# Kernel tuning notes

Measured on AMD Instinct MI355X. Metric: run time of the kernel, lower is better.

## Reference

```python
import jax, jax.numpy as jnp
import numpy as np

BS, N, D, B, D_PM = 8, 4096, 1024, 8, 64
BUDGET = 16.0


def setup_inputs() -> dict:
    key = jax.random.key(0)
    ks = jax.random.split(key, 6)
    H = jax.random.normal(ks[0], (BS, N, D), jnp.float32)
    surprise = jax.random.normal(ks[1], (BS, N, D), jnp.float32)
    # W_pm initialized as (1/B)*I + small noise, as in initialize()
    eye = jnp.eye(D_PM, dtype=jnp.float32)
    W_pm = eye / B + 0.01 * jax.random.normal(ks[2], (BS, B, D_PM, D_PM), jnp.float32)
    proj_in_w = jax.random.normal(ks[3], (D_PM, D), jnp.float32) / np.float32(np.sqrt(D))
    proj_in_b = jnp.zeros((D_PM,), jnp.float32)
    # original zero-inits proj_out; use small values so output is non-trivial
    proj_out_w = 0.02 * jax.random.normal(ks[4], (D, D_PM), jnp.float32)
    proj_out_b = jnp.zeros((D,), jnp.float32)
    raw_beta = jnp.full((B,), -3.0, jnp.float32)
    raw_decay = jnp.full((B,), np.float32(np.log(0.999 / 0.001)), jnp.float32)  # logit(0.999)
    surp_scale = jnp.ones((1,), jnp.float32)
    surp_bias = jnp.zeros((1,), jnp.float32)
    return dict(H=H, surprise=surprise, W_pm=W_pm,
                proj_in_w=proj_in_w, proj_in_b=proj_in_b,
                proj_out_w=proj_out_w, proj_out_b=proj_out_b,
                raw_beta=raw_beta, raw_decay=raw_decay,
                surp_scale=surp_scale, surp_bias=surp_bias)


def reference(H, surprise, W_pm, proj_in_w, proj_in_b, proj_out_w, proj_out_b,
              raw_beta, raw_decay, surp_scale, surp_bias):
    # ---- read ----
    pre = jnp.einsum('bnd,pd->bnp', H, proj_in_w) + proj_in_b          # [BS,N,D_pm]
    W_sum = jnp.sum(W_pm, axis=1)                                      # [BS,D_pm,D_pm]
    post = jnp.einsum('bnp,bqp->bnq', pre, W_sum)                      # pre @ W_sum^T
    pm_read = jnp.einsum('bnq,dq->bnd', post, proj_out_w) + proj_out_b # [BS,N,D]
    # ---- commit (Hebbian, surprise-gated) ----
    surp_mag = jnp.linalg.norm(surprise, axis=-1)                      # [BS,N]
    s = jax.nn.sigmoid(surp_scale * surp_mag + surp_bias)              # [BS,N]
    weighted = jnp.sqrt(s)[..., None] * pre                            # [BS,N,D_pm]
    G = jnp.einsum('bnp,bnq->bpq', weighted, weighted) / N             # [BS,D_pm,D_pm]
    beta = jax.nn.softplus(raw_beta)                                   # [B]
    decay = jax.nn.sigmoid(raw_decay)                                  # [B]
    eye = jnp.eye(D_PM, dtype=pre.dtype)
    T = decay[None, :, None, None] * eye + beta[None, :, None, None] * G[:, None]  # [BS,B,D_pm,D_pm]
    W_new = jnp.einsum('bkij,bkjq->bkiq', W_pm, T)                     # [BS,B,D_pm,D_pm]
    frob = jnp.sqrt(jnp.sum(W_new * W_new, axis=(-2, -1), keepdims=True))
    scale = jnp.minimum(BUDGET / jnp.maximum(frob, 1e-8), 1.0)
    W_new = W_new * scale
    return pm_read, W_new
```

## Files before the change

kernel.cpp:

```cpp
#include <hip/hip_runtime.h>

typedef unsigned short u16;
typedef unsigned int u32;
typedef __attribute__((ext_vector_type(4))) float f32x4;
typedef __attribute__((ext_vector_type(8))) short s16x8;

static constexpr int N_ = 4096;
static constexpr int D_ = 1024;

#define WAITV(N) asm volatile("s_waitcnt vmcnt(" #N ")" ::: "memory")
#define MEMCLOB() asm volatile("" ::: "memory")

__device__ __forceinline__ u16 f2bf(float f) {
  unsigned u = __float_as_uint(f);
  u += 0x7FFFu + ((u >> 16) & 1u);
  return (u16)(u >> 16);
}

__device__ __forceinline__ f32x4 zero4() {
  f32x4 z; z[0] = 0.f; z[1] = 0.f; z[2] = 0.f; z[3] = 0.f; return z;
}

__device__ __forceinline__ void gload16(const void* g, void* lds) {
  __builtin_amdgcn_global_load_lds(
      (const __attribute__((address_space(1))) u32*)g,
      (__attribute__((address_space(3))) u32*)lds, 16, 0, 0);
}

__global__ __launch_bounds__(256) void k_aux(
    const float* __restrict__ Wpm, const float* __restrict__ piw,
    const float* __restrict__ pw, u16* __restrict__ WpB,
    u16* __restrict__ MB) {
  __shared__ float Ws[64][65];
  int bid = blockIdx.x, tid = threadIdx.x;
  if (bid < 16) {
    size_t i0 = (size_t)bid * 4096;
    for (int idx = tid; idx < 4096; idx += 256)
      WpB[i0 + idx] = f2bf(piw[i0 + idx]);
    return;
  }
  int idx2 = bid - 16;
  int b = idx2 >> 4, t = idx2 & 15;
  for (int idx = tid; idx < 4096; idx += 256) {
    float s = 0.f;
#pragma unroll
    for (int k = 0; k < 8; ++k)
      s += Wpm[((size_t)(b * 8 + k)) * 4096 + idx];
    Ws[idx >> 6][idx & 63] = s;
  }
  __syncthreads();
  u16* mb = MB + ((size_t)b << 16);
  for (int oidx = tid; oidx < 4096; oidx += 256) {
    int r = oidx >> 6, c = oidx & 63;
    int drow = t * 64 + r;
    const float* prow = pw + (size_t)drow * 64;
    float acc = 0.f;
#pragma unroll 8
    for (int q = 0; q < 64; ++q) acc += prow[q] * Ws[q][c];
    mb[(size_t)drow * 64 + c] = f2bf(acc);
  }
}

__global__ __launch_bounds__(512, 4) void k_main(
    const float* __restrict__ H, const float* __restrict__ Sur,
    const float* __restrict__ pib, const float* __restrict__ pob,
    const float* __restrict__ sscale_p, const float* __restrict__ sbias_p,
    const u16* __restrict__ WpB, const u16* __restrict__ MB,
    float* __restrict__ Gpart, float* __restrict__ out) {
  __shared__ __align__(16) char arena[65536];
  __shared__ float sqsL[64];

  const int tid = threadIdx.x;
  const int lane = tid & 63;
  const int w = tid >> 6;
  const int wm = w & 3;
  const int wk = w >> 2;
  const int llo = lane & 15;
  const int lhi = lane >> 4;
  const int b = blockIdx.x >> 6;
  const int row0 = (blockIdx.x & 63) * 64;

  {
    const float* sb = Sur + ((size_t)b * N_ + row0) * D_;
    const float sscale = sscale_p[0], sbias = sbias_p[0];
#pragma unroll
    for (int g = 0; g < 2; ++g) {
      const float4* r0 = (const float4*)(sb + (size_t)(w * 8 + g * 4) * D_) + lane;
      float s0 = 0.f, s1 = 0.f, s2 = 0.f, s3 = 0.f;
#pragma unroll
      for (int c = 0; c < 4; ++c) {
        float4 v0 = r0[c * 64];
        float4 v1 = r0[256 + c * 64];
        float4 v2 = r0[512 + c * 64];
        float4 v3 = r0[768 + c * 64];
        s0 += v0.x * v0.x + v0.y * v0.y + v0.z * v0.z + v0.w * v0.w;
        s1 += v1.x * v1.x + v1.y * v1.y + v1.z * v1.z + v1.w * v1.w;
        s2 += v2.x * v2.x + v2.y * v2.y + v2.z * v2.z + v2.w * v2.w;
        s3 += v3.x * v3.x + v3.y * v3.y + v3.z * v3.z + v3.w * v3.w;
      }
#pragma unroll
      for (int m = 1; m < 64; m <<= 1) {
        s0 += __shfl_xor(s0, m, 64);
        s1 += __shfl_xor(s1, m, 64);
        s2 += __shfl_xor(s2, m, 64);
        s3 += __shfl_xor(s3, m, 64);
      }
      float res = s0;
      if (lane == 1) res = s1;
      if (lane == 2) res = s2;
      if (lane == 3) res = s3;
      if (lane < 4) {
        float mag = sqrtf(res);
        float s = 1.f / (1.f + __expf(-(sscale * mag + sbias)));
        sqsL[w * 8 + g * 4 + lane] = sqrtf(s);
      }
    }
  }
  __syncthreads();

  const int srow = 8 * w + (lane >> 3);
  const int sc16 = (lane & 7) ^ (srow & 7);
  const float* hsrc = H + ((size_t)b * N_ + row0 + srow) * D_ + sc16 * 4;
  const u16* wpb = WpB + (size_t)wk * 512 + lhi * 8;

  f32x4 accA[4];
#pragma unroll
  for (int t = 0; t < 4; ++t) accA[t] = zero4();
  s16x8 Bf[2][4];

  const int arow = wm * 16 + llo;
  const int r7a = arow & 7;

#define STAGEH(kc)                                                          \
  gload16(hsrc + (kc) * 32, arena + ((kc) & 3) * 16384 + w * 1024);         \
  gload16(hsrc + 512 + (kc) * 32, arena + ((kc) & 3) * 16384 + 8192 + w * 1024)

#define LOADB(kc)                                                           \
  _Pragma("unroll") for (int t = 0; t < 4; ++t) Bf[(kc) & 1][t] =           \
      *(const s16x8*)(wpb + (size_t)(t * 16 + llo) * 1024 + (kc) * 32)

  STAGEH(0); STAGEH(1); STAGEH(2);
  LOADB(0); LOADB(1);
  MEMCLOB();

#pragma unroll
  for (int kc = 0; kc < 16; ++kc) {
    if (kc <= 13) { WAITV(12); }
    else if (kc == 14) { WAITV(8); }
    else { WAITV(0); }
    __builtin_amdgcn_s_barrier();
    MEMCLOB();
    {
      const char* abase = arena + (kc & 3) * 16384 + wk * 8192 + arow * 128;
      f32x4 alo = *(const f32x4*)(abase + (((lhi * 2) ^ r7a) * 16));
      f32x4 ahi = *(const f32x4*)(abase + (((lhi * 2 + 1) ^ r7a) * 16));
      s16x8 af;
      af[0] = (short)f2bf(alo[0]); af[1] = (short)f2bf(alo[1]);
      af[2] = (short)f2bf(alo[2]); af[3] = (short)f2bf(alo[3]);
      af[4] = (short)f2bf(ahi[0]); af[5] = (short)f2bf(ahi[1]);
      af[6] = (short)f2bf(ahi[2]); af[7] = (short)f2bf(ahi[3]);
#pragma unroll
      for (int t = 0; t < 4; ++t)
        accA[t] = __builtin_amdgcn_mfma_f32_16x16x32_bf16(af, Bf[kc & 1][t],
                                                          accA[t], 0, 0, 0);
    }
    if (kc + 2 < 16) { LOADB(kc + 2); }
    if (kc + 3 < 16) { STAGEH(kc + 3); }
    MEMCLOB();
  }
#undef STAGEH
#undef LOADB

  float bias_t[4];
#pragma unroll
  for (int t = 0; t < 4; ++t) bias_t[t] = pib[t * 16 + llo];

  __syncthreads();
  float (*preF)[65] = (float(*)[65])arena;
  u16 (*preRP)[72] = (u16(*)[72])(arena + 18432);
  u16 (*wRPT)[72] = (u16(*)[72])(arena + 28672);
  float* pobL = (float*)(arena + 38912);

  if (wk == 1) {
#pragma unroll
    for (int t = 0; t < 4; ++t)
#pragma unroll
      for (int r = 0; r < 4; ++r)
        preF[wm * 16 + lhi * 4 + r][t * 16 + llo] = accA[t][r];
  }
  __syncthreads();
  if (wk == 0) {
#pragma unroll
    for (int t = 0; t < 4; ++t)
#pragma unroll
      for (int r = 0; r < 4; ++r) {
        int row = wm * 16 + lhi * 4 + r;
        float v = accA[t][r] + preF[row][t * 16 + llo] + bias_t[t];
        preRP[row][t * 16 + llo] = f2bf(v);
        wRPT[t * 16 + llo][row] = f2bf(v * sqsL[row]);
      }
  }
  __syncthreads();

  {
    f32x4 accG[4];
#pragma unroll
    for (int t = 0; t < 4; ++t) accG[t] = zero4();
    s16x8 ag = *(const s16x8*)&wRPT[wm * 16 + llo][wk * 32 + lhi * 8];
#pragma unroll
    for (int t = 0; t < 4; ++t) {
      s16x8 bg = *(const s16x8*)&wRPT[t * 16 + llo][wk * 32 + lhi * 8];
      accG[t] = __builtin_amdgcn_mfma_f32_16x16x32_bf16(ag, bg, accG[t], 0, 0, 0);
    }
    float* gout = Gpart + ((size_t)blockIdx.x * 2 + wk) * 4096;
#pragma unroll
    for (int t = 0; t < 4; ++t)
#pragma unroll
      for (int r = 0; r < 4; ++r)
        gout[(wm * 16 + lhi * 4 + r) * 64 + t * 16 + llo] = accG[t][r];
  }
  pobL[tid] = pob[tid];
  pobL[tid + 512] = pob[tid + 512];
  __syncthreads();

  {
    s16x8 ad0 = *(const s16x8*)&preRP[wm * 16 + llo][lhi * 8];
    s16x8 ad1 = *(const s16x8*)&preRP[wm * 16 + llo][32 + lhi * 8];
    const u16* mcol = MB + ((size_t)b << 16) + (size_t)(wk * 512) * 64 + lhi * 8;
    float* orow = out + ((size_t)b * N_ + row0 + wm * 16) * D_;
#pragma unroll
    for (int c = 0; c < 8; ++c) {
      s16x8 f0[4], f1[4];
#pragma unroll
      for (int i = 0; i < 4; ++i) {
        const u16* p = mcol + (size_t)(c * 64 + i * 16 + llo) * 64;
        f0[i] = *(const s16x8*)p;
        f1[i] = *(const s16x8*)(p + 32);
      }
#pragma unroll
      for (int i = 0; i < 4; ++i) {
        f32x4 acc = zero4();
        acc = __builtin_amdgcn_mfma_f32_16x16x32_bf16(ad0, f0[i], acc, 0, 0, 0);
        acc = __builtin_amdgcn_mfma_f32_16x16x32_bf16(ad1, f1[i], acc, 0, 0, 0);
        int n0 = wk * 512 + c * 64 + i * 16;
        float bias = pobL[n0 + llo];
#pragma unroll
        for (int r = 0; r < 4; ++r)
          orow[(size_t)(lhi * 4 + r) * D_ + n0 + llo] = acc[r] + bias;
      }
    }
  }
}

__global__ __launch_bounds__(256) void k_gred(
    const float* __restrict__ Gpart, float* __restrict__ Gsum) {
  __shared__ float red[4][64];
  int b = blockIdx.x >> 6, g = blockIdx.x & 63;
  int lane = threadIdx.x & 63, q = threadIdx.x >> 6;
  const float* src = Gpart + ((size_t)b * 128 + q * 32) * 4096 + g * 64 + lane;
  float s = 0.f;
#pragma unroll 8
  for (int i = 0; i < 32; ++i) s += src[(size_t)i * 4096];
  red[q][lane] = s;
  __syncthreads();
  if (q == 0)
    Gsum[(size_t)b * 4096 + g * 64 + lane] =
        red[0][lane] + red[1][lane] + red[2][lane] + red[3][lane];
}

__global__ __launch_bounds__(256) void k_wnew(
    const float* __restrict__ Wpm, const float* __restrict__ Gsum,
    const float* __restrict__ rbeta, const float* __restrict__ rdecay,
    float* __restrict__ outW) {
  __shared__ float Wk[64][66];
  __shared__ float Gl[64][66];
  __shared__ float red[4];
  int bk = blockIdx.x;
  int b = bk >> 3, k = bk & 7;
  int tid = threadIdx.x;
  const float* wsrc = Wpm + (size_t)bk * 4096;
  const float* gsrc = Gsum + (size_t)b * 4096;
  for (int idx = tid; idx < 4096; idx += 256) {
    Wk[idx >> 6][idx & 63] = wsrc[idx];
    Gl[idx >> 6][idx & 63] = gsrc[idx];
  }
  __syncthreads();
  float beta = log1pf(__expf(rbeta[k]));
  float decay = 1.f / (1.f + __expf(-rdecay[k]));
  float bn = beta * (1.f / 4096.f);
  int q = tid & 63;
  int rbase = tid >> 6;
  float vals[16];
  float ss = 0.f;
#pragma unroll
  for (int i = 0; i < 16; ++i) {
    int row = i * 4 + rbase;
    float acc = 0.f;
#pragma unroll 8
    for (int j = 0; j < 64; ++j) acc += Wk[row][j] * Gl[j][q];
    float v = decay * Wk[row][q] + bn * acc;
    vals[i] = v;
    ss += v * v;
  }
#pragma unroll
  for (int m = 1; m < 64; m <<= 1) ss += __shfl_xor(ss, m, 64);
  if ((tid & 63) == 0) red[tid >> 6] = ss;
  __syncthreads();
  float frob = sqrtf(red[0] + red[1] + red[2] + red[3]);
  float scale = fminf(16.f / fmaxf(frob, 1e-8f), 1.f);
  float* dst = outW + (size_t)bk * 4096;
#pragma unroll
  for (int i = 0; i < 16; ++i) dst[i * 256 + tid] = vals[i] * scale;
}

extern "C" void kernel_launch(void* const* d_in, const int* in_sizes, int n_in,
                              void* d_out, int out_size, void* d_ws, size_t ws_size,
                              hipStream_t stream) {
  const float* H      = (const float*)d_in[0];
  const float* Sur    = (const float*)d_in[1];
  const float* Wpm    = (const float*)d_in[2];
  const float* piw    = (const float*)d_in[3];
  const float* pib    = (const float*)d_in[4];
  const float* pw     = (const float*)d_in[5];
  const float* pob    = (const float*)d_in[6];
  const float* rbeta  = (const float*)d_in[7];
  const float* rdecay = (const float*)d_in[8];
  const float* sscale = (const float*)d_in[9];
  const float* sbias  = (const float*)d_in[10];
  float* out = (float*)d_out;

  char* ws = (char*)d_ws;
  u16* WpB     = (u16*)(ws);
  u16* MB      = (u16*)(ws + 131072);
  float* Gsum  = (float*)(ws + 1179648);
  float* Gpart = (float*)(ws + 1310720);

  k_aux<<<144, 256, 0, stream>>>(Wpm, piw, pw, WpB, MB);
  k_main<<<512, 512, 0, stream>>>(H, Sur, pib, pob, sscale, sbias,
                                  WpB, MB, Gpart, out);
  k_gred<<<512, 256, 0, stream>>>(Gpart, Gsum);
  k_wnew<<<64, 256, 0, stream>>>(Wpm, Gsum, rbeta, rdecay,
                                 out + (size_t)8 * 4096 * 1024);
}
```

Before: 164.6 us.

## Move surprise-norm gating into aux kernel and make H staging per-wave barrier-free

The surprise row-norm and sigmoid gate move out of the main GEMM kernel into extra blocks of the auxiliary kernel, which write per-row sqrt(s) to workspace. The main kernel then starts H streaming immediately and reads four gate values per lane. H staging is restructured so each wave loads exactly the rows and k-half it consumes into its own LDS slice, which removes the per-iteration workgroup barrier. The trade-off is a workspace round trip for the gate values and a larger aux launch that runs serially before the main kernel.

```diff
diff --git a/kernel.cpp b/kernel.cpp
--- a/kernel.cpp
+++ b/kernel.cpp
@@ -29,8 +29,9 @@
 
 __global__ __launch_bounds__(256) void k_aux(
     const float* __restrict__ Wpm, const float* __restrict__ piw,
-    const float* __restrict__ pw, u16* __restrict__ WpB,
-    u16* __restrict__ MB) {
+    const float* __restrict__ pw, const float* __restrict__ Sur,
+    const float* __restrict__ sscale_p, const float* __restrict__ sbias_p,
+    u16* __restrict__ WpB, u16* __restrict__ MB, float* __restrict__ sqs_ws) {
   __shared__ float Ws[64][65];
   int bid = blockIdx.x, tid = threadIdx.x;
   if (bid < 16) {
@@ -39,36 +40,68 @@
       WpB[i0 + idx] = f2bf(piw[i0 + idx]);
     return;
   }
-  int idx2 = bid - 16;
-  int b = idx2 >> 4, t = idx2 & 15;
-  for (int idx = tid; idx < 4096; idx += 256) {
-    float s = 0.f;
-#pragma unroll
-    for (int k = 0; k < 8; ++k)
-      s += Wpm[((size_t)(b * 8 + k)) * 4096 + idx];
-    Ws[idx >> 6][idx & 63] = s;
-  }
-  __syncthreads();
-  u16* mb = MB + ((size_t)b << 16);
-  for (int oidx = tid; oidx < 4096; oidx += 256) {
-    int r = oidx >> 6, c = oidx & 63;
-    int drow = t * 64 + r;
-    const float* prow = pw + (size_t)drow * 64;
-    float acc = 0.f;
+  if (bid < 144) {
+    int idx2 = bid - 16;
+    int b = idx2 >> 4, t = idx2 & 15;
+    for (int idx = tid; idx < 4096; idx += 256) {
+      float s = 0.f;
+#pragma unroll
+      for (int k = 0; k < 8; ++k)
+        s += Wpm[((size_t)(b * 8 + k)) * 4096 + idx];
+      Ws[idx >> 6][idx & 63] = s;
+    }
+    __syncthreads();
+    u16* mb = MB + ((size_t)b << 16);
+    for (int oidx = tid; oidx < 4096; oidx += 256) {
+      int r = oidx >> 6, c = oidx & 63;
+      int drow = t * 64 + r;
+      const float* prow = pw + (size_t)drow * 64;
+      float acc = 0.f;
 #pragma unroll 8
-    for (int q = 0; q < 64; ++q) acc += prow[q] * Ws[q][c];
-    mb[(size_t)drow * 64 + c] = f2bf(acc);
+      for (int q = 0; q < 64; ++q) acc += prow[q] * Ws[q][c];
+      mb[(size_t)drow * 64 + c] = f2bf(acc);
+    }
+    return;
+  }
+  int w = tid >> 6, lane = tid & 63;
+  int fr = (bid - 144) * 16 + w * 4;
+  const float4* r0 = (const float4*)(Sur + (size_t)fr * 1024) + lane;
+  float s0 = 0.f, s1 = 0.f, s2 = 0.f, s3 = 0.f;
+#pragma unroll
+  for (int c = 0; c < 4; ++c) {
+    float4 v0 = r0[c * 64];
+    float4 v1 = r0[256 + c * 64];
+    float4 v2 = r0[512 + c * 64];
+    float4 v3 = r0[768 + c * 64];
+    s0 += v0.x * v0.x + v0.y * v0.y + v0.z * v0.z + v0.w * v0.w;
+    s1 += v1.x * v1.x + v1.y * v1.y + v1.z * v1.z + v1.w * v1.w;
+    s2 += v2.x * v2.x + v2.y * v2.y + v2.z * v2.z + v2.w * v2.w;
+    s3 += v3.x * v3.x + v3.y * v3.y + v3.z * v3.z + v3.w * v3.w;
+  }
+#pragma unroll
+  for (int m = 1; m < 64; m <<= 1) {
+    s0 += __shfl_xor(s0, m, 64);
+    s1 += __shfl_xor(s1, m, 64);
+    s2 += __shfl_xor(s2, m, 64);
+    s3 += __shfl_xor(s3, m, 64);
+  }
+  float res = s0;
+  if (lane == 1) res = s1;
+  if (lane == 2) res = s2;
+  if (lane == 3) res = s3;
+  if (lane < 4) {
+    float mag = sqrtf(res);
+    float s = 1.f / (1.f + __expf(-(sscale_p[0] * mag + sbias_p[0])));
+    sqs_ws[fr + lane] = sqrtf(s);
   }
 }
 
 __global__ __launch_bounds__(512, 4) void k_main(
-    const float* __restrict__ H, const float* __restrict__ Sur,
-    const float* __restrict__ pib, const float* __restrict__ pob,
-    const float* __restrict__ sscale_p, const float* __restrict__ sbias_p,
-    const u16* __restrict__ WpB, const u16* __restrict__ MB,
+    const float* __restrict__ H, const float* __restrict__ pib,
+    const float* __restrict__ pob, const u16* __restrict__ WpB,
+    const u16* __restrict__ MB, const float* __restrict__ sqs_ws,
     float* __restrict__ Gpart, float* __restrict__ out) {
   __shared__ __align__(16) char arena[65536];
-  __shared__ float sqsL[64];
 
   const int tid = threadIdx.x;
   const int lane = tid & 63;
@@ -80,47 +113,19 @@
   const int b = blockIdx.x >> 6;
   const int row0 = (blockIdx.x & 63) * 64;
 
-  {
-    const float* sb = Sur + ((size_t)b * N_ + row0) * D_;
-    const float sscale = sscale_p[0], sbias = sbias_p[0];
-#pragma unroll
-    for (int g = 0; g < 2; ++g) {
-      const float4* r0 = (const float4*)(sb + (size_t)(w * 8 + g * 4) * D_) + lane;
-      float s0 = 0.f, s1 = 0.f, s2 = 0.f, s3 = 0.f;
-#pragma unroll
-      for (int c = 0; c < 4; ++c) {
-        float4 v0 = r0[c * 64];
-        float4 v1 = r0[256 + c * 64];
-        float4 v2 = r0[512 + c * 64];
-        float4 v3 = r0[768 + c * 64];
-        s0 += v0.x * v0.x + v0.y * v0.y + v0.z * v0.z + v0.w * v0.w;
-        s1 += v1.x * v1.x + v1.y * v1.y + v1.z * v1.z + v1.w * v1.w;
-        s2 += v2.x * v2.x + v2.y * v2.y + v2.z * v2.z + v2.w * v2.w;
-        s3 += v3.x * v3.x + v3.y * v3.y + v3.z * v3.z + v3.w * v3.w;
-      }
-#pragma unroll
-      for (int m = 1; m < 64; m <<= 1) {
-        s0 += __shfl_xor(s0, m, 64);
-        s1 += __shfl_xor(s1, m, 64);
-        s2 += __shfl_xor(s2, m, 64);
-        s3 += __shfl_xor(s3, m, 64);
-      }
-      float res = s0;
-      if (lane == 1) res = s1;
-      if (lane == 2) res = s2;
-      if (lane == 3) res = s3;
-      if (lane < 4) {
-        float mag = sqrtf(res);
-        float s = 1.f / (1.f + __expf(-(sscale * mag + sbias)));
-        sqsL[w * 8 + g * 4 + lane] = sqrtf(s);
-      }
-    }
-  }
-  __syncthreads();
-
-  const int srow = 8 * w + (lane >> 3);
-  const int sc16 = (lane & 7) ^ (srow & 7);
-  const float* hsrc = H + ((size_t)b * N_ + row0 + srow) * D_ + sc16 * 4;
+  float bias_t[4];
+#pragma unroll
+  for (int t = 0; t < 4; ++t) bias_t[t] = pib[t * 16 + llo];
+  float sqs_r[4];
+#pragma unroll
+  for (int r = 0; r < 4; ++r)
+    sqs_r[r] = sqs_ws[b * 4096 + row0 + wm * 16 + lhi * 4 + r];
+
+  const int c16 = (lane & 7) ^ (lane >> 3);
+  const float* hsrc0 = H + ((size_t)b * N_ + row0 + wm * 16 + (lane >> 3)) * D_ +
+                       wk * 512 + c16 * 4;
+  const float* hsrc1 = hsrc0 + 8 * D_;
+  char* wbase = arena + w * 2048;
   const u16* wpb = WpB + (size_t)wk * 512 + lhi * 8;
 
   f32x4 accA[4];
@@ -128,32 +133,34 @@
   for (int t = 0; t < 4; ++t) accA[t] = zero4();
   s16x8 Bf[2][4];
 
-  const int arow = wm * 16 + llo;
-  const int r7a = arow & 7;
-
-#define STAGEH(kc)                                                          \
-  gload16(hsrc + (kc) * 32, arena + ((kc) & 3) * 16384 + w * 1024);         \
-  gload16(hsrc + 512 + (kc) * 32, arena + ((kc) & 3) * 16384 + 8192 + w * 1024)
-
-#define LOADB(kc)                                                           \
-  _Pragma("unroll") for (int t = 0; t < 4; ++t) Bf[(kc) & 1][t] =           \
+#define STAGEH(kc)                                                     \
+  gload16(hsrc0 + (kc) * 32, wbase + ((kc) & 3) * 16384);              \
+  gload16(hsrc1 + (kc) * 32, wbase + ((kc) & 3) * 16384 + 1024)
+
+#define LOADB(kc)                                                      \
+  _Pragma("unroll") for (int t = 0; t < 4; ++t) Bf[(kc) & 1][t] =      \
       *(const s16x8*)(wpb + (size_t)(t * 16 + llo) * 1024 + (kc) * 32)
 
-  STAGEH(0); STAGEH(1); STAGEH(2);
-  LOADB(0); LOADB(1);
-  MEMCLOB();
+  STAGEH(0); MEMCLOB();
+  LOADB(0);  MEMCLOB();
+  STAGEH(1); MEMCLOB();
+  LOADB(1);  MEMCLOB();
+  STAGEH(2); MEMCLOB();
+
+  const int jblk = (llo >> 3) * 1024;
+  const int r7 = llo & 7;
+  const int slot_lo = r7 * 8 + ((lhi * 2) ^ r7);
+  const int slot_hi = r7 * 8 + ((lhi * 2 + 1) ^ r7);
 
 #pragma unroll
   for (int kc = 0; kc < 16; ++kc) {
-    if (kc <= 13) { WAITV(12); }
-    else if (kc == 14) { WAITV(8); }
+    if (kc <= 13) { WAITV(8); }
+    else if (kc == 14) { WAITV(6); }
     else { WAITV(0); }
-    __builtin_amdgcn_s_barrier();
-    MEMCLOB();
     {
-      const char* abase = arena + (kc & 3) * 16384 + wk * 8192 + arow * 128;
-      f32x4 alo = *(const f32x4*)(abase + (((lhi * 2) ^ r7a) * 16));
-      f32x4 ahi = *(const f32x4*)(abase + (((lhi * 2 + 1) ^ r7a) * 16));
+      const char* base = arena + (kc & 3) * 16384 + w * 2048 + jblk;
+      f32x4 alo = *(const f32x4*)(base + slot_lo * 16);
+      f32x4 ahi = *(const f32x4*)(base + slot_hi * 16);
       s16x8 af;
       af[0] = (short)f2bf(alo[0]); af[1] = (short)f2bf(alo[1]);
       af[2] = (short)f2bf(alo[2]); af[3] = (short)f2bf(alo[3]);
@@ -164,16 +171,14 @@
         accA[t] = __builtin_amdgcn_mfma_f32_16x16x32_bf16(af, Bf[kc & 1][t],
                                                           accA[t], 0, 0, 0);
     }
+    MEMCLOB();
     if (kc + 2 < 16) { LOADB(kc + 2); }
+    MEMCLOB();
     if (kc + 3 < 16) { STAGEH(kc + 3); }
     MEMCLOB();
   }
 #undef STAGEH
 #undef LOADB
-
-  float bias_t[4];
-#pragma unroll
-  for (int t = 0; t < 4; ++t) bias_t[t] = pib[t * 16 + llo];
 
   __syncthreads();
   float (*preF)[65] = (float(*)[65])arena;
@@ -197,7 +202,7 @@
         int row = wm * 16 + lhi * 4 + r;
         float v = accA[t][r] + preF[row][t * 16 + llo] + bias_t[t];
         preRP[row][t * 16 + llo] = f2bf(v);
-        wRPT[t * 16 + llo][row] = f2bf(v * sqsL[row]);
+        wRPT[t * 16 + llo][row] = f2bf(v * sqs_r[r]);
       }
   }
   __syncthreads();
@@ -330,14 +335,15 @@
   float* out = (float*)d_out;
 
   char* ws = (char*)d_ws;
-  u16* WpB     = (u16*)(ws);
-  u16* MB      = (u16*)(ws + 131072);
-  float* Gsum  = (float*)(ws + 1179648);
-  float* Gpart = (float*)(ws + 1310720);
-
-  k_aux<<<144, 256, 0, stream>>>(Wpm, piw, pw, WpB, MB);
-  k_main<<<512, 512, 0, stream>>>(H, Sur, pib, pob, sscale, sbias,
-                                  WpB, MB, Gpart, out);
+  u16* WpB      = (u16*)(ws);
+  u16* MB       = (u16*)(ws + 131072);
+  float* sqs_ws = (float*)(ws + 1179648);
+  float* Gsum   = (float*)(ws + 1310720);
+  float* Gpart  = (float*)(ws + 1441792);
+
+  k_aux<<<2192, 256, 0, stream>>>(Wpm, piw, pw, Sur, sscale, sbias,
+                                  WpB, MB, sqs_ws);
+  k_main<<<512, 512, 0, stream>>>(H, pib, pob, WpB, MB, sqs_ws, Gpart, out);
   k_gred<<<512, 256, 0, stream>>>(Gpart, Gsum);
   k_wnew<<<64, 256, 0, stream>>>(Wpm, Gsum, rbeta, rdecay,
                                  out + (size_t)8 * 4096 * 1024);
```

Result: faster. 160.9 us (-2.3%).
